# Optimization experiments

Measured on AMD Instinct MI355X. Metric: run time of the kernel, lower is better.

The kernel has to match this reference:

```python
import jax, jax.numpy as jnp
import numpy as np

NBINS = 10001  # hardcoded in the torch module (10000*sigmoid in [0,10000])


def setup_inputs() -> dict:
    key = jax.random.key(0)
    k1, k2 = jax.random.split(key)
    N = 33554432  # 2**25 samples
    preds = jax.random.normal(k1, (N,), dtype=jnp.float32)
    targets = jax.random.randint(k2, (N,), 0, 2).astype(jnp.float32)
    return {"preds": preds, "targets": targets}


def reference(preds, targets):
    # y_pred = int(10000 * sigmoid(preds)); truncation == floor since value >= 0
    y_pred = (10000.0 * jax.nn.sigmoid(preds)).reshape(-1).astype(jnp.int32)
    y_true = targets.reshape(-1)
    is_pos = (y_true >= 0.5).astype(preds.dtype)
    # scatter-add histogram split by label (single pass, atomic-add style)
    tpi = jnp.zeros((NBINS,), dtype=preds.dtype).at[y_pred].add(is_pos)
    fpi = jnp.zeros((NBINS,), dtype=preds.dtype).at[y_pred].add(1.0 - is_pos)
    # KS statistic: max |CDF_pos - CDF_neg|
    tp_cum = jnp.cumsum(tpi)
    fp_cum = jnp.cumsum(fpi)
    tp_curve = tp_cum / tp_cum[-1]
    fp_curve = fp_cum / fp_cum[-1]
    return jnp.max(jnp.abs(tp_curve - fp_curve))
```

## Files before the change

kernel.cpp:

```cpp
#include <hip/hip_runtime.h>

#define NBINS 10001
#define ROWP  10016
#define HIST_BLOCKS 768
#define HIST_THREADS 512
#define PCHUNK 128

typedef unsigned int u32;
typedef unsigned long long u64;
typedef float f4 __attribute__((ext_vector_type(4)));

__device__ __forceinline__ f4 ntload(const f4* p) {
    return __builtin_nontemporal_load(p);
}

__device__ __forceinline__ int ks_bin(float x) {
    float e = __expf(-x);
    float s = __builtin_amdgcn_rcpf(1.0f + e);
    int b = (int)(10000.0f * s);
    b = b < 0 ? 0 : b;
    return b > 10000 ? 10000 : b;
}

__device__ __forceinline__ void ks_acc4(u32* lh, f4 p, f4 t) {
#pragma unroll
    for (int k = 0; k < 4; ++k) {
        int b = ks_bin(p[k]);
        u32 add = (t[k] >= 0.5f) ? 0x10000u : 1u;
        atomicAdd(&lh[b], add);
    }
}

__global__ __launch_bounds__(HIST_THREADS) void ks_hist(
        const float* __restrict__ preds, const float* __restrict__ tgts,
        u64* __restrict__ ghist, u32* __restrict__ partials,
        int use_partials, int n) {
    __shared__ u32 lh[NBINS];
    for (int i = threadIdx.x; i < NBINS; i += HIST_THREADS) lh[i] = 0u;
    __syncthreads();

    const int n4 = n >> 2;
    const f4* p4 = (const f4*)preds;
    const f4* t4 = (const f4*)tgts;
    const int tid = blockIdx.x * HIST_THREADS + threadIdx.x;
    const int stride = gridDim.x * HIST_THREADS;

    int i = tid;
    for (; i + 3 * stride < n4; i += 4 * stride) {
        f4 p0 = ntload(p4 + i);
        f4 t0 = ntload(t4 + i);
        f4 p1 = ntload(p4 + i + stride);
        f4 t1 = ntload(t4 + i + stride);
        f4 p2 = ntload(p4 + i + 2 * stride);
        f4 t2 = ntload(t4 + i + 2 * stride);
        f4 p3 = ntload(p4 + i + 3 * stride);
        f4 t3 = ntload(t4 + i + 3 * stride);
        ks_acc4(lh, p0, t0);
        ks_acc4(lh, p1, t1);
        ks_acc4(lh, p2, t2);
        ks_acc4(lh, p3, t3);
    }
    for (; i < n4; i += stride) {
        f4 p = ntload(p4 + i);
        f4 t = ntload(t4 + i);
        ks_acc4(lh, p, t);
    }

    if (blockIdx.x == 0) {
        int base = n4 << 2;
        int rem = n - base;
        if ((int)threadIdx.x < rem) {
            int j = base + threadIdx.x;
            int b = ks_bin(preds[j]);
            u32 add = (tgts[j] >= 0.5f) ? 0x10000u : 1u;
            atomicAdd(&lh[b], add);
        }
    }
    __syncthreads();

    if (use_partials) {
        u32* mypart = partials + (size_t)blockIdx.x * ROWP;
        for (int b = threadIdx.x; b < NBINS; b += HIST_THREADS)
            mypart[b] = lh[b];
    } else {
        for (int b = threadIdx.x; b < NBINS; b += HIST_THREADS) {
            u32 v = lh[b];
            if (v) {
                u64 a = ((u64)(v >> 16) << 32) | (u64)(v & 0xFFFFu);
                atomicAdd(&ghist[b], a);
            }
        }
    }
}

__global__ __launch_bounds__(256) void ks_reduce(const u32* __restrict__ partials,
                                                 u64* __restrict__ ghist) {
    int bin = blockIdx.x * 256 + threadIdx.x;
    if (bin >= NBINS) return;
    const u32* base = partials + (size_t)blockIdx.y * PCHUNK * ROWP + bin;
    u32 tp = 0, fp = 0;
#pragma unroll 4
    for (int k = 0; k < PCHUNK; ++k) {
        u32 v = base[(size_t)k * ROWP];
        tp += v >> 16;
        fp += v & 0xFFFFu;
    }
    atomicAdd(&ghist[bin], ((u64)tp << 32) | (u64)fp);
}

__global__ __launch_bounds__(1024) void ks_scan(const u64* __restrict__ ghist,
                                                float* __restrict__ out) {
    __shared__ long long stp[1024];
    __shared__ long long sfp[1024];
    __shared__ double smx[1024];

    const int t = threadIdx.x;
    const int CH = 10;
    const int lo = t * CH;

    u64 loc[CH];
    long long tps = 0, fps = 0;
#pragma unroll
    for (int k = 0; k < CH; ++k) {
        int i = lo + k;
        u64 v = (i < NBINS) ? ghist[i] : 0ull;
        loc[k] = v;
        tps += (long long)(v >> 32);
        fps += (long long)(v & 0xFFFFFFFFull);
    }
    stp[t] = tps;
    sfp[t] = fps;
    __syncthreads();

    for (int off = 1; off < 1024; off <<= 1) {
        long long a = stp[t], b = sfp[t];
        long long c = 0, d = 0;
        if (t >= off) { c = stp[t - off]; d = sfp[t - off]; }
        __syncthreads();
        stp[t] = a + c;
        sfp[t] = b + d;
        __syncthreads();
    }

    const long long TP = stp[1023];
    const long long FP = sfp[1023];
    const long long etp = stp[t] - tps;
    const long long efp = sfp[t] - fps;

    const double invTP = 1.0 / (double)(TP > 0 ? TP : 1);
    const double invFP = 1.0 / (double)(FP > 0 ? FP : 1);

    double m = 0.0;
    long long tc = etp, fc = efp;
#pragma unroll
    for (int k = 0; k < CH; ++k) {
        u64 v = loc[k];
        tc += (long long)(v >> 32);
        fc += (long long)(v & 0xFFFFFFFFull);
        double d = fabs((double)tc * invTP - (double)fc * invFP);
        m = (d > m) ? d : m;
    }

    smx[t] = m;
    __syncthreads();
    for (int off = 512; off > 0; off >>= 1) {
        if (t < off) smx[t] = smx[t] > smx[t + off] ? smx[t] : smx[t + off];
        __syncthreads();
    }
    if (t == 0) out[0] = (float)smx[0];
}

extern "C" void kernel_launch(void* const* d_in, const int* in_sizes, int n_in,
                              void* d_out, int out_size, void* d_ws, size_t ws_size,
                              hipStream_t stream) {
    const float* preds = (const float*)d_in[0];
    const float* tgts  = (const float*)d_in[1];
    const int n = in_sizes[0];

    const size_t part_off = 131072;
    const size_t need = part_off + (size_t)HIST_BLOCKS * ROWP * sizeof(u32);
    u64* ghist = (u64*)d_ws;
    u32* partials = (u32*)((char*)d_ws + part_off);
    const int use_partials = (ws_size >= need) ? 1 : 0;

    hipMemsetAsync(d_ws, 0, NBINS * sizeof(u64), stream);

    ks_hist<<<HIST_BLOCKS, HIST_THREADS, 0, stream>>>(preds, tgts, ghist,
                                                      partials, use_partials, n);
    if (use_partials) {
        dim3 rg((NBINS + 255) / 256, HIST_BLOCKS / PCHUNK);
        ks_reduce<<<rg, 256, 0, stream>>>(partials, ghist);
    }
    ks_scan<<<1, 1024, 0, stream>>>(ghist, (float*)d_out);
}
```

Baseline: 80.85 us.

## Drop memset and atomics in reduce, use plain loads in histogram

The reduce kernel now has each thread sum all 768 partial rows for its bin and write the result directly, replacing the 2D grid with atomic adds. This lets the host skip the workspace memset when partials are used. Nontemporal loads in the histogram kernel become ordinary loads. Only 40 blocks now run the reduce, each thread doing a long serial strided read, which may leave the GPU underused compared with the previous 240-block grid.

```diff
diff --git a/kernel.cpp b/kernel.cpp
--- a/kernel.cpp
+++ b/kernel.cpp
@@ -4,15 +4,10 @@
 #define ROWP  10016
 #define HIST_BLOCKS 768
 #define HIST_THREADS 512
-#define PCHUNK 128
 
 typedef unsigned int u32;
 typedef unsigned long long u64;
 typedef float f4 __attribute__((ext_vector_type(4)));
-
-__device__ __forceinline__ f4 ntload(const f4* p) {
-    return __builtin_nontemporal_load(p);
-}
 
 __device__ __forceinline__ int ks_bin(float x) {
     float e = __expf(-x);
@@ -47,22 +42,22 @@
 
     int i = tid;
     for (; i + 3 * stride < n4; i += 4 * stride) {
-        f4 p0 = ntload(p4 + i);
-        f4 t0 = ntload(t4 + i);
-        f4 p1 = ntload(p4 + i + stride);
-        f4 t1 = ntload(t4 + i + stride);
-        f4 p2 = ntload(p4 + i + 2 * stride);
-        f4 t2 = ntload(t4 + i + 2 * stride);
-        f4 p3 = ntload(p4 + i + 3 * stride);
-        f4 t3 = ntload(t4 + i + 3 * stride);
+        f4 p0 = p4[i];
+        f4 t0 = t4[i];
+        f4 p1 = p4[i + stride];
+        f4 t1 = t4[i + stride];
+        f4 p2 = p4[i + 2 * stride];
+        f4 t2 = t4[i + 2 * stride];
+        f4 p3 = p4[i + 3 * stride];
+        f4 t3 = t4[i + 3 * stride];
         ks_acc4(lh, p0, t0);
         ks_acc4(lh, p1, t1);
         ks_acc4(lh, p2, t2);
         ks_acc4(lh, p3, t3);
     }
     for (; i < n4; i += stride) {
-        f4 p = ntload(p4 + i);
-        f4 t = ntload(t4 + i);
+        f4 p = p4[i];
+        f4 t = t4[i];
         ks_acc4(lh, p, t);
     }
 
@@ -97,15 +92,15 @@
                                                  u64* __restrict__ ghist) {
     int bin = blockIdx.x * 256 + threadIdx.x;
     if (bin >= NBINS) return;
-    const u32* base = partials + (size_t)blockIdx.y * PCHUNK * ROWP + bin;
+    const u32* base = partials + bin;
     u32 tp = 0, fp = 0;
-#pragma unroll 4
-    for (int k = 0; k < PCHUNK; ++k) {
+#pragma unroll 8
+    for (int k = 0; k < HIST_BLOCKS; ++k) {
         u32 v = base[(size_t)k * ROWP];
         tp += v >> 16;
         fp += v & 0xFFFFu;
     }
-    atomicAdd(&ghist[bin], ((u64)tp << 32) | (u64)fp);
+    ghist[bin] = ((u64)tp << 32) | (u64)fp;
 }
 
 __global__ __launch_bounds__(1024) void ks_scan(const u64* __restrict__ ghist,
@@ -183,13 +178,13 @@
     u32* partials = (u32*)((char*)d_ws + part_off);
     const int use_partials = (ws_size >= need) ? 1 : 0;
 
-    hipMemsetAsync(d_ws, 0, NBINS * sizeof(u64), stream);
+    if (!use_partials)
+        hipMemsetAsync(d_ws, 0, NBINS * sizeof(u64), stream);
 
     ks_hist<<<HIST_BLOCKS, HIST_THREADS, 0, stream>>>(preds, tgts, ghist,
                                                       partials, use_partials, n);
     if (use_partials) {
-        dim3 rg((NBINS + 255) / 256, HIST_BLOCKS / PCHUNK);
-        ks_reduce<<<rg, 256, 0, stream>>>(partials, ghist);
+        ks_reduce<<<(NBINS + 255) / 256, 256, 0, stream>>>(partials, ghist);
     }
     ks_scan<<<1, 1024, 0, stream>>>(ghist, (float*)d_out);
 }
```

After: 83.06 us. +2.7%, slower.
